# Kernel optimization log

Hardware: AMD Instinct MI355X
Metric: run time of the kernel (lower is better)

Reference implementation:

```python
import jax, jax.numpy as jnp
import numpy as np

V, D, H, L_GNN = 50000, 256, 256, 4
B, NODES_PER_G, L, OUT = 16, 4000, 512, 256
N = B * NODES_PER_G            # 64000 total nodes
E = N * 16                     # 1,024,000 edges (avg degree 16)


def setup_inputs() -> dict:
    key = jax.random.key(0)
    ks = jax.random.split(key, 14)
    s = 0.02  # param init scale
    # per-graph local indices, offset into the flat node array (mirrors the
    # indices[...] + sum(x_len[:i]) reconstruction in the torch code)
    local = jax.random.randint(ks[3], (B, L), 0, NODES_PER_G)
    offsets = (jnp.arange(B, dtype=jnp.int32) * NODES_PER_G)[:, None]
    return {
        "x": jax.random.randint(ks[0], (N,), 0, V, dtype=jnp.int32),
        "edge_index": jax.random.randint(ks[1], (2, E), 0, N, dtype=jnp.int32),
        "edge_weight": jax.random.uniform(ks[2], (E,), jnp.float32),
        "gather_idx": (local + offsets).astype(jnp.int32),
        "mask": jnp.ones((B, L), dtype=bool),
        "encoder_embed": jax.random.normal(ks[4], (B, L, H), jnp.float32),
        "emb": jax.random.normal(ks[5], (V, D), jnp.float32) * s,
        "ggc_w": jax.random.normal(ks[6], (L_GNN, H, H), jnp.float32) * s,
        "w_ih": jax.random.normal(ks[7], (3 * H, H), jnp.float32) * s,
        "w_hh": jax.random.normal(ks[8], (3 * H, H), jnp.float32) * s,
        "b_ih": jnp.zeros((3 * H,), jnp.float32),
        "b_hh": jnp.zeros((3 * H,), jnp.float32),
        "out_w": jax.random.normal(ks[9], (OUT, 2 * H), jnp.float32) * s,
        "out_b": jnp.zeros((OUT,), jnp.float32),
    }


def _gru_cell(m, h, w_ih, w_hh, b_ih, b_hh):
    # torch.nn.GRUCell, gate order (r, z, n)
    gi = m @ w_ih.T + b_ih          # [N, 3H]
    gh = h @ w_hh.T + b_hh
    i_r, i_z, i_n = jnp.split(gi, 3, axis=-1)
    h_r, h_z, h_n = jnp.split(gh, 3, axis=-1)
    r = jax.nn.sigmoid(i_r + h_r)
    z = jax.nn.sigmoid(i_z + h_z)
    n = jnp.tanh(i_n + r * h_n)
    return (1.0 - z) * n + z * h


def reference(x, edge_index, edge_weight, gather_idx, mask, encoder_embed,
              emb, ggc_w, w_ih, w_hh, b_ih, b_hh, out_w, out_b):
    src, dst = edge_index[0], edge_index[1]  # PyG: aggregate x_j at target i
    h = emb[x]                                # [N, H] (dropout=0 -> identity)
    for i in range(L_GNN):                    # GatedGraphConv
        m = h @ ggc_w[i]                      # [N, H]
        msg = m[src] * edge_weight[:, None]   # [E, H]
        agg = jax.ops.segment_sum(msg, dst, num_segments=N)
        h = _gru_cell(agg, h, w_ih, w_hh, b_ih, b_hh)
    # gather per-graph node outputs and zero-pad to max_node_len
    out = h[gather_idx] * mask[:, :, None].astype(h.dtype)  # [B, L, H]
    out = jnp.concatenate([out, encoder_embed], axis=-1)    # [B, L, 2H]
    return out @ out_w.T + out_b                            # [B, L, OUT]
```

## Files before the change

kernel.cpp:

```cpp
#include <hip/hip_runtime.h>
#include <hip/hip_bf16.h>

typedef __hip_bfloat16 bf16;
typedef unsigned short u16;
typedef __attribute__((ext_vector_type(8))) short s8v;
typedef __attribute__((ext_vector_type(4))) float f4v;

#define MFMA16(a, b, c) __builtin_amdgcn_mfma_f32_16x16x32_bf16((a), (b), (c), 0, 0, 0)

__device__ __forceinline__ float b2f(bf16 v) { return __bfloat162float(v); }
__device__ __forceinline__ float sigm(float x) {
  return __builtin_amdgcn_rcpf(1.0f + __expf(-x));
}
__device__ __forceinline__ float ftanh(float x) {
  return __builtin_fmaf(2.f, sigm(2.f * x), -1.f);
}
__device__ __forceinline__ float u2f(u16 u) {
  union { float f; unsigned int i; } v; v.i = ((unsigned int)u) << 16; return v.f;
}
__device__ __forceinline__ u16 f2u(float f) {
  bf16 b = __float2bfloat16(f);
  union { bf16 b; u16 u; } v; v.b = b; return v.u;
}

__device__ __forceinline__ void gl16(void* lds, const void* g) {
  __builtin_amdgcn_global_load_lds(
      (const __attribute__((address_space(1))) unsigned int*)g,
      (__attribute__((address_space(3))) unsigned int*)lds, 16, 0, 0);
}

__global__ __launch_bounds__(256) void k_cast4(const float* __restrict__ s0,
                                               const float* __restrict__ s1,
                                               const float* __restrict__ s2,
                                               const float* __restrict__ s3,
                                               bf16* __restrict__ d0,
                                               bf16* __restrict__ d1,
                                               bf16* __restrict__ d2,
                                               bf16* __restrict__ d3,
                                               int q0, int q1, int q2, int q3) {
  int i = blockIdx.x * 256 + threadIdx.x;
  const float* s; bf16* d;
  if (i < q0)            { s = s0; d = d0; }
  else if ((i -= q0) < q1) { s = s1; d = d1; }
  else if ((i -= q1) < q2) { s = s2; d = d2; }
  else if ((i -= q2) < q3) { s = s3; d = d3; }
  else return;
  float4 v = *(const float4*)(s + (size_t)i * 4);
  ushort4 o;
  o.x = f2u(v.x); o.y = f2u(v.y); o.z = f2u(v.z); o.w = f2u(v.w);
  *(ushort4*)((u16*)d + (size_t)i * 4) = o;
}

__global__ __launch_bounds__(256) void k_embed(const int* __restrict__ x,
                                               const float* __restrict__ emb,
                                               bf16* __restrict__ h, int N, int H) {
  int idx = blockIdx.x * 256 + threadIdx.x;
  int hq = H >> 2;
  if (idx >= N * hq) return;
  int n = idx / hq, c4 = idx - n * hq;
  float4 v = *(const float4*)(emb + (size_t)x[n] * H + c4 * 4);
  ushort4 o;
  o.x = f2u(v.x); o.y = f2u(v.y); o.z = f2u(v.z); o.w = f2u(v.w);
  *(ushort4*)((u16*)h + (size_t)idx * 4) = o;
}

__global__ __launch_bounds__(256) void k_cat(const bf16* __restrict__ h,
                                             const int* __restrict__ gidx,
                                             const float* __restrict__ enc,
                                             bf16* __restrict__ catA, int BL, int H) {
  int i = blockIdx.x * 256 + threadIdx.x;
  if (i >= BL * 2 * H) return;
  int r = i / (2 * H), k = i - r * 2 * H;
  catA[i] = (k < H) ? h[(size_t)gidx[r] * H + k]
                    : __float2bfloat16(enc[(size_t)r * H + (k - H)]);
}

__global__ __launch_bounds__(256) void k_zero_i32(int* __restrict__ p, int n) {
  int i = blockIdx.x * 256 + threadIdx.x;
  if (i < n) p[i] = 0;
}
__global__ __launch_bounds__(256) void k_hist(const int* __restrict__ ei,
                                              int* __restrict__ deg, int E) {
  int e = blockIdx.x * 256 + threadIdx.x;
  if (e < E) atomicAdd(&deg[ei[E + e]], 1);
}

__global__ __launch_bounds__(256) void k_scan1(const int* __restrict__ deg,
                                               int* __restrict__ bsum, int N) {
  int t = threadIdx.x;
  int i = blockIdx.x * 256 + t;
  int v = (i < N) ? deg[i] : 0;
#pragma unroll
  for (int o = 32; o > 0; o >>= 1) v += __shfl_down(v, o, 64);
  __shared__ int ws[4];
  if ((t & 63) == 0) ws[t >> 6] = v;
  __syncthreads();
  if (t == 0) bsum[blockIdx.x] = ws[0] + ws[1] + ws[2] + ws[3];
}
__global__ __launch_bounds__(256) void k_scan2(const int* __restrict__ bsum,
                                               int* __restrict__ boff, int nb) {
  __shared__ int s[256];
  int t = threadIdx.x;
  int carry = 0;
  for (int base = 0; base < nb; base += 256) {
    int v = (base + t < nb) ? bsum[base + t] : 0;
    s[t] = v;
    __syncthreads();
    for (int o = 1; o < 256; o <<= 1) {
      int u = (t >= o) ? s[t - o] : 0;
      __syncthreads();
      s[t] += u;
      __syncthreads();
    }
    if (base + t < nb) boff[base + t] = carry + s[t] - v;
    carry += s[255];
    __syncthreads();
  }
}
__global__ __launch_bounds__(256) void k_scan3(const int* __restrict__ deg,
                                               const int* __restrict__ boff,
                                               int* __restrict__ rowptr,
                                               int* __restrict__ cursor, int N) {
  __shared__ int s[256];
  int t = threadIdx.x;
  int i = blockIdx.x * 256 + t;
  int v = (i < N) ? deg[i] : 0;
  s[t] = v;
  __syncthreads();
  for (int o = 1; o < 256; o <<= 1) {
    int u = (t >= o) ? s[t - o] : 0;
    __syncthreads();
    s[t] += u;
    __syncthreads();
  }
  int ex = boff[blockIdx.x] + s[t] - v;
  if (i < N) { rowptr[i] = ex; cursor[i] = ex; }
  if (i == N - 1) rowptr[N] = ex + v;
}

__global__ __launch_bounds__(256) void k_fill(const int* __restrict__ ei,
                                              const float* __restrict__ ew,
                                              int* __restrict__ cursor,
                                              int2* __restrict__ ef, int E) {
  int e = blockIdx.x * 256 + threadIdx.x;
  if (e >= E) return;
  int d = ei[E + e];
  int pos = atomicAdd(&cursor[d], 1);
  ef[pos] = make_int2(ei[e], __float_as_int(ew[e]));
}

__global__ __launch_bounds__(256) void k_aggregate(const int* __restrict__ rowptr,
                                                   const int2* __restrict__ ef,
                                                   const bf16* __restrict__ hsrc,
                                                   bf16* __restrict__ sh,
                                                   int N, int H) {
  int wv = threadIdx.x >> 6, lane = threadIdx.x & 63;
  int d = blockIdx.x * 4 + wv;
  if (d >= N) return;
  int beg = rowptr[d], end = rowptr[d + 1];
  int half = lane >> 5;
  const u16* hp = (const u16*)hsrc;
  for (int c0 = (lane & 31) * 8; c0 < H; c0 += 256) {
    float f0 = 0.f, f1 = 0.f, f2 = 0.f, f3 = 0.f;
    float f4 = 0.f, f5 = 0.f, f6 = 0.f, f7 = 0.f;
    int i = beg;
    for (; i + 8 <= end; i += 8) {
      int2 eA = ef[i + half],     eB = ef[i + 2 + half];
      int2 eC = ef[i + 4 + half], eD = ef[i + 6 + half];
      float wA = __int_as_float(eA.y), wB = __int_as_float(eB.y);
      float wC = __int_as_float(eC.y), wD = __int_as_float(eD.y);
      s8v rA = *(const s8v*)(hp + (size_t)eA.x * H + c0);
      s8v rB = *(const s8v*)(hp + (size_t)eB.x * H + c0);
      s8v rC = *(const s8v*)(hp + (size_t)eC.x * H + c0);
      s8v rD = *(const s8v*)(hp + (size_t)eD.x * H + c0);
      f0 += wA * u2f((u16)rA[0]) + wB * u2f((u16)rB[0]) + wC * u2f((u16)rC[0]) + wD * u2f((u16)rD[0]);
      f1 += wA * u2f((u16)rA[1]) + wB * u2f((u16)rB[1]) + wC * u2f((u16)rC[1]) + wD * u2f((u16)rD[1]);
      f2 += wA * u2f((u16)rA[2]) + wB * u2f((u16)rB[2]) + wC * u2f((u16)rC[2]) + wD * u2f((u16)rD[2]);
      f3 += wA * u2f((u16)rA[3]) + wB * u2f((u16)rB[3]) + wC * u2f((u16)rC[3]) + wD * u2f((u16)rD[3]);
      f4 += wA * u2f((u16)rA[4]) + wB * u2f((u16)rB[4]) + wC * u2f((u16)rC[4]) + wD * u2f((u16)rD[4]);
      f5 += wA * u2f((u16)rA[5]) + wB * u2f((u16)rB[5]) + wC * u2f((u16)rC[5]) + wD * u2f((u16)rD[5]);
      f6 += wA * u2f((u16)rA[6]) + wB * u2f((u16)rB[6]) + wC * u2f((u16)rC[6]) + wD * u2f((u16)rD[6]);
      f7 += wA * u2f((u16)rA[7]) + wB * u2f((u16)rB[7]) + wC * u2f((u16)rC[7]) + wD * u2f((u16)rD[7]);
    }
    for (; i + 2 <= end; i += 2) {
      int2 eA = ef[i + half];
      float wA = __int_as_float(eA.y);
      s8v rA = *(const s8v*)(hp + (size_t)eA.x * H + c0);
      f0 += wA * u2f((u16)rA[0]); f1 += wA * u2f((u16)rA[1]);
      f2 += wA * u2f((u16)rA[2]); f3 += wA * u2f((u16)rA[3]);
      f4 += wA * u2f((u16)rA[4]); f5 += wA * u2f((u16)rA[5]);
      f6 += wA * u2f((u16)rA[6]); f7 += wA * u2f((u16)rA[7]);
    }
    if (i < end && half == 0) {
      int2 eA = ef[i];
      float wA = __int_as_float(eA.y);
      s8v rA = *(const s8v*)(hp + (size_t)eA.x * H + c0);
      f0 += wA * u2f((u16)rA[0]); f1 += wA * u2f((u16)rA[1]);
      f2 += wA * u2f((u16)rA[2]); f3 += wA * u2f((u16)rA[3]);
      f4 += wA * u2f((u16)rA[4]); f5 += wA * u2f((u16)rA[5]);
      f6 += wA * u2f((u16)rA[6]); f7 += wA * u2f((u16)rA[7]);
    }
    f0 += __shfl_xor(f0, 32); f1 += __shfl_xor(f1, 32);
    f2 += __shfl_xor(f2, 32); f3 += __shfl_xor(f3, 32);
    f4 += __shfl_xor(f4, 32); f5 += __shfl_xor(f5, 32);
    f6 += __shfl_xor(f6, 32); f7 += __shfl_xor(f7, 32);
    if (half == 0) {
      s8v o;
      o[0] = (short)f2u(f0); o[1] = (short)f2u(f1);
      o[2] = (short)f2u(f2); o[3] = (short)f2u(f3);
      o[4] = (short)f2u(f4); o[5] = (short)f2u(f5);
      o[6] = (short)f2u(f6); o[7] = (short)f2u(f7);
      *(s8v*)((u16*)sh + (size_t)d * H + c0) = o;
    }
  }
}

template <int OUT_F32>
__global__ __launch_bounds__(256) void k_gemm(const bf16* __restrict__ A,
                                              const bf16* __restrict__ Bt,
                                              void* __restrict__ Cv,
                                              const float* __restrict__ bias,
                                              int M, int K, int Nc,
                                              size_t sBt, size_t sC) {
  __shared__ short As[128][40];
  __shared__ short Bs[64][40];
  int gm = blockIdx.x * 128, gn = blockIdx.y * 64;
  Bt += (size_t)blockIdx.z * sBt;
  size_t zc = (size_t)blockIdx.z * sC;
  int tid = threadIdx.x, w = tid >> 6, lane = tid & 63;
  int l15 = lane & 15, koff = (lane >> 4) * 8;
  f4v acc[2][4];
#pragma unroll
  for (int i = 0; i < 2; i++)
#pragma unroll
    for (int j = 0; j < 4; j++) acc[i][j] = (f4v)0.f;

  for (int kt = 0; kt < K; kt += 32) {
#pragma unroll
    for (int c = 0; c < 2; c++) {
      int ch = tid + c * 256;
      int row = ch >> 2, seg = ch & 3;
      *(float4*)&As[row][seg * 8] =
          *(const float4*)(A + (size_t)(gm + row) * K + kt + seg * 8);
    }
    {
      int row = tid >> 2, seg = tid & 3;
      *(float4*)&Bs[row][seg * 8] =
          *(const float4*)(Bt + (size_t)(gn + row) * K + kt + seg * 8);
    }
    __syncthreads();
    s8v af[2], bf[4];
#pragma unroll
    for (int rt = 0; rt < 2; rt++) af[rt] = *(const s8v*)&As[w * 32 + rt * 16 + l15][koff];
#pragma unroll
    for (int ct = 0; ct < 4; ct++) bf[ct] = *(const s8v*)&Bs[ct * 16 + l15][koff];
#pragma unroll
    for (int rt = 0; rt < 2; rt++)
#pragma unroll
      for (int ct = 0; ct < 4; ct++) acc[rt][ct] = MFMA16(af[rt], bf[ct], acc[rt][ct]);
    __syncthreads();
  }
#pragma unroll
  for (int rt = 0; rt < 2; rt++)
#pragma unroll
    for (int ct = 0; ct < 4; ct++)
#pragma unroll
      for (int r = 0; r < 4; r++) {
        int row = gm + w * 32 + rt * 16 + (lane >> 4) * 4 + r;
        int col = gn + ct * 16 + l15;
        float v = acc[rt][ct][r];
        if (OUT_F32) ((float*)Cv)[zc + (size_t)row * Nc + col] = v + bias[col];
        else         ((bf16*)Cv)[zc + (size_t)row * Nc + col] = __float2bfloat16(v);
      }
}

#define GRU_STAGE(Aarr, Harr, Barr, kt)                   \
  {                                                       \
    gl16(&Aarr[tid * 8],            Ap  + (kt));          \
    gl16(&Aarr[2048 + tid * 8],     Ap  + rstep + (kt));  \
    gl16(&Harr[tid * 8],            Hp  + (kt));          \
    gl16(&Harr[2048 + tid * 8],     Hp  + rstep + (kt));  \
    gl16(&Barr[tid * 8],            BiP + (kt));          \
    gl16(&Barr[2048 + tid * 8],     BiP + HH + (kt));     \
    gl16(&Barr[2 * 2048 + tid * 8], BiP + 2 * HH + (kt)); \
    gl16(&Barr[3 * 2048 + tid * 8], BhP + (kt));          \
    gl16(&Barr[4 * 2048 + tid * 8], BhP + HH + (kt));     \
    gl16(&Barr[5 * 2048 + tid * 8], BhP + 2 * HH + (kt)); \
  }

#define GRU_COMPUTE(Aarr, Harr, Barr)                                       \
  {                                                                         \
    s8v fa[2], fh[2];                                                       \
    _Pragma("unroll")                                                       \
    for (int rt = 0; rt < 2; rt++) {                                        \
      fa[rt] = *(const s8v*)&Aarr[(w * 32 + rt * 16 + l15) * 32 + koff];    \
      fh[rt] = *(const s8v*)&Harr[(w * 32 + rt * 16 + l15) * 32 + koff];    \
    }                                                                       \
    _Pragma("unroll")                                                       \
    for (int ct = 0; ct < 4; ct++) {                                        \
      int brow = (ct * 16 + l15) * 32 + koff;                               \
      s8v bRi = *(const s8v*)&Barr[brow];                                   \
      s8v bZi = *(const s8v*)&Barr[2048 + brow];                            \
      s8v bNi = *(const s8v*)&Barr[2 * 2048 + brow];                        \
      s8v bRh = *(const s8v*)&Barr[3 * 2048 + brow];                        \
      s8v bZh = *(const s8v*)&Barr[4 * 2048 + brow];                        \
      s8v bNh = *(const s8v*)&Barr[5 * 2048 + brow];                        \
      _Pragma("unroll")                                                     \
      for (int rt = 0; rt < 2; rt++) {                                      \
        accR[rt][ct]  = MFMA16(fa[rt], bRi, accR[rt][ct]);                  \
        accR[rt][ct]  = MFMA16(fh[rt], bRh, accR[rt][ct]);                  \
        accZ[rt][ct]  = MFMA16(fa[rt], bZi, accZ[rt][ct]);                  \
        accZ[rt][ct]  = MFMA16(fh[rt], bZh, accZ[rt][ct]);                  \
        accNi[rt][ct] = MFMA16(fa[rt], bNi, accNi[rt][ct]);                 \
        accNh[rt][ct] = MFMA16(fh[rt], bNh, accNh[rt][ct]);                 \
      }                                                                     \
    }                                                                       \
  }

__global__ __launch_bounds__(256, 2) void k_gru_mfma(const bf16* __restrict__ Ash,
                                                     const bf16* __restrict__ Ah,
                                                     const bf16* __restrict__ Wi,
                                                     const bf16* __restrict__ Wh,
                                                     const float* __restrict__ bi,
                                                     const float* __restrict__ bh,
                                                     bf16* __restrict__ hn,
                                                     int M, int H) {
  __shared__ __align__(16) short Aa0[128 * 32], Aa1[128 * 32];
  __shared__ __align__(16) short Hs0[128 * 32], Hs1[128 * 32];
  __shared__ __align__(16) short Bs0[6 * 64 * 32], Bs1[6 * 64 * 32];

  int nwgx = H >> 6;
  int nwg = gridDim.x;
  int bid = blockIdx.x;
  int wg = bid;
  if ((nwg & 7) == 0) { int cpx = nwg >> 3; wg = (bid & 7) * cpx + (bid >> 3); }
  int gcol = (wg % nwgx) * 64;
  int gm = (wg / nwgx) * 128;

  int tid = threadIdx.x, w = tid >> 6, lane = tid & 63;
  int l15 = lane & 15, koff = (lane >> 4) * 8;
  f4v accR[2][4], accZ[2][4], accNi[2][4], accNh[2][4];
#pragma unroll
  for (int rt = 0; rt < 2; rt++)
#pragma unroll
    for (int ct = 0; ct < 4; ct++) {
      accR[rt][ct] = (f4v)0.f; accZ[rt][ct] = (f4v)0.f;
      accNi[rt][ct] = (f4v)0.f; accNh[rt][ct] = (f4v)0.f;
    }

  int arow = tid >> 2, aseg = tid & 3;
  const bf16* Ap  = Ash + (size_t)(gm + arow) * H + aseg * 8;
  const bf16* Hp  = Ah  + (size_t)(gm + arow) * H + aseg * 8;
  const bf16* BiP = Wi  + (size_t)(gcol + arow) * H + aseg * 8;
  const bf16* BhP = Wh  + (size_t)(gcol + arow) * H + aseg * 8;
  size_t HH = (size_t)H * H;
  size_t rstep = (size_t)64 * H;

  int nk = H >> 5;
  GRU_STAGE(Aa0, Hs0, Bs0, 0);
  __syncthreads();
  for (int t = 0; t < nk; t += 2) {
    int kt = t << 5;
    if (t + 1 < nk) GRU_STAGE(Aa1, Hs1, Bs1, kt + 32);
    GRU_COMPUTE(Aa0, Hs0, Bs0);
    __syncthreads();
    if (t + 2 < nk) GRU_STAGE(Aa0, Hs0, Bs0, kt + 64);
    if (t + 1 < nk) GRU_COMPUTE(Aa1, Hs1, Bs1);
    __syncthreads();
  }

#pragma unroll
  for (int ct = 0; ct < 4; ct++) {
    int col = gcol + ct * 16 + l15;
    float br  = bi[col] + bh[col];
    float bz  = bi[H + col] + bh[H + col];
    float bin = bi[2 * H + col], bhn = bh[2 * H + col];
#pragma unroll
    for (int rt = 0; rt < 2; rt++)
#pragma unroll
      for (int r = 0; r < 4; r++) {
        int row = gm + w * 32 + rt * 16 + (lane >> 4) * 4 + r;
        float rr = sigm(accR[rt][ct][r] + br);
        float zz = sigm(accZ[rt][ct][r] + bz);
        float nn = ftanh(accNi[rt][ct][r] + bin + rr * (accNh[rt][ct][r] + bhn));
        float hv = b2f(Ah[(size_t)row * H + col]);
        hn[(size_t)row * H + col] = __float2bfloat16((1.f - zz) * nn + zz * hv);
      }
  }
}

static inline size_t alg(size_t x) { return (x + 255) & ~(size_t)255; }
static inline int cdiv(int a, int b) { return (a + b - 1) / b; }

extern "C" void kernel_launch(void* const* d_in, const int* in_sizes, int n_in,
                              void* d_out, int out_size, void* d_ws, size_t ws_size,
                              hipStream_t stream) {
  (void)out_size; (void)ws_size;
  int s = (n_in >= 14) ? 0 : -1;
  const int*   x     = (const int*)d_in[0];
  const int*   ei    = (const int*)d_in[1];
  const float* ew    = (const float*)d_in[2];
  const int*   gidx  = (const int*)d_in[3];
  const float* enc   = (const float*)d_in[5 + s];
  const float* emb   = (const float*)d_in[6 + s];
  const float* ggcw  = (const float*)d_in[7 + s];
  const float* w_ih  = (const float*)d_in[8 + s];
  const float* w_hh  = (const float*)d_in[9 + s];
  const float* b_ih  = (const float*)d_in[10 + s];
  const float* b_hh  = (const float*)d_in[11 + s];
  const float* out_w = (const float*)d_in[12 + s];
  const float* out_b = (const float*)d_in[13 + s];
  float* out = (float*)d_out;

  int N   = in_sizes[0];
  int E   = in_sizes[2];
  int BL  = in_sizes[3];
  int H   = in_sizes[5 + s] / BL;
  int LG  = in_sizes[7 + s] / (H * H);
  int OUT = in_sizes[12 + s] / (2 * H);

  size_t nh = (size_t)N * H;
  size_t hh3 = (size_t)3 * H * H;
  int nb = cdiv(N, 256);
  char* p = (char*)d_ws;
  size_t off = 0;
  bf16* wihB  = (bf16*)(p + off); off = alg(off + hh3 * 2);
  bf16* whhB  = (bf16*)(p + off); off = alg(off + hh3 * 2);
  bf16* outwB = (bf16*)(p + off); off = alg(off + (size_t)OUT * 2 * H * 2);
  bf16* ggcwB = (bf16*)(p + off); off = alg(off + (size_t)LG * H * H * 2);
  bf16* Ucomb = (bf16*)(p + off); off = alg(off + (size_t)LG * hh3 * 2);
  bf16* hA    = (bf16*)(p + off); off = alg(off + nh * 2);
  bf16* hB    = (bf16*)(p + off); off = alg(off + nh * 2);
  bf16* shB   = (bf16*)(p + off); off = alg(off + nh * 2);
  bf16* catA  = (bf16*)(p + off); off = alg(off + (size_t)BL * 2 * H * 2);
  int* deg    = (int*)(p + off);  off = alg(off + (size_t)N * 4);
  int* rowptr = (int*)(p + off);  off = alg(off + (size_t)(N + 1) * 4);
  int* cursor = (int*)(p + off);  off = alg(off + (size_t)N * 4);
  int2* ef    = (int2*)(p + off); off = alg(off + (size_t)E * 8);
  int* bsum   = (int*)(p + off);  off = alg(off + (size_t)nb * 4);
  int* boff   = (int*)(p + off);  off = alg(off + (size_t)nb * 4);

  int q0 = (int)(hh3 >> 2), q1 = q0, q2 = (OUT * 2 * H) >> 2,
      q3 = (LG * H * H) >> 2;
  k_cast4<<<cdiv(q0 + q1 + q2 + q3, 256), 256, 0, stream>>>(
      w_ih, w_hh, out_w, ggcw, wihB, whhB, outwB, ggcwB, q0, q1, q2, q3);
  k_gemm<0><<<dim3(3 * H / 128, H / 64, LG), 256, 0, stream>>>(
      wihB, ggcwB, Ucomb, nullptr, 3 * H, H, H, (size_t)H * H, hh3);

  k_embed<<<cdiv(N * (H >> 2), 256), 256, 0, stream>>>(x, emb, hA, N, H);
  k_zero_i32<<<cdiv(N, 256), 256, 0, stream>>>(deg, N);
  k_hist<<<cdiv(E, 256), 256, 0, stream>>>(ei, deg, E);
  k_scan1<<<nb, 256, 0, stream>>>(deg, bsum, N);
  k_scan2<<<1, 256, 0, stream>>>(bsum, boff, nb);
  k_scan3<<<nb, 256, 0, stream>>>(deg, boff, rowptr, cursor, N);
  k_fill<<<cdiv(E, 256), 256, 0, stream>>>(ei, ew, cursor, ef, E);

  bf16* h = hA;
  bf16* hn = hB;
  for (int l = 0; l < LG; l++) {
    k_aggregate<<<cdiv(N, 4), 256, 0, stream>>>(rowptr, ef, h, shB, N, H);
    k_gru_mfma<<<dim3((H / 64) * (N / 128)), 256, 0, stream>>>(
        shB, h, Ucomb + (size_t)l * hh3, whhB, b_ih, b_hh, hn, N, H);
    bf16* t = h; h = hn; hn = t;
  }
  k_cat<<<cdiv(BL * 2 * H, 256), 256, 0, stream>>>(h, gidx, enc, catA, BL, H);
  k_gemm<1><<<dim3(BL / 128, OUT / 64, 1), 256, 0, stream>>>(
      catA, outwB, out, out_b, BL, 2 * H, OUT, 0, 0);
}
```

Before: 822.8 us.

## Fuse embed, weight cast and degree zeroing; partition CSR atomics by dst range

Merges the embedding gather, the weight casts and the degree-buffer zeroing into one prep kernel, removing two launches. The histogram and fill kernels now use a fixed grid of 2048 blocks split into 8 destination ranges. Each block scans its slice of the edge list but only issues atomics for destinations in its own range. The aim is to localise atomic traffic to a slice of deg and cursor so it stays in cache, at the cost of each edge index being read 8 times.

New measurement: 795.1 us. 1.03x faster.

```diff
diff --git a/kernel.cpp b/kernel.cpp
--- a/kernel.cpp
+++ b/kernel.cpp
@@ -29,39 +29,46 @@
       (__attribute__((address_space(3))) unsigned int*)lds, 16, 0, 0);
 }
 
-__global__ __launch_bounds__(256) void k_cast4(const float* __restrict__ s0,
-                                               const float* __restrict__ s1,
-                                               const float* __restrict__ s2,
-                                               const float* __restrict__ s3,
-                                               bf16* __restrict__ d0,
-                                               bf16* __restrict__ d1,
-                                               bf16* __restrict__ d2,
-                                               bf16* __restrict__ d3,
-                                               int q0, int q1, int q2, int q3) {
+__global__ __launch_bounds__(256) void k_prep(const int* __restrict__ x,
+                                              const float* __restrict__ emb,
+                                              bf16* __restrict__ h,
+                                              const float* __restrict__ s0,
+                                              const float* __restrict__ s1,
+                                              const float* __restrict__ s2,
+                                              const float* __restrict__ s3,
+                                              bf16* __restrict__ d0,
+                                              bf16* __restrict__ d1,
+                                              bf16* __restrict__ d2,
+                                              bf16* __restrict__ d3,
+                                              int q0, int q1, int q2, int q3,
+                                              int4* __restrict__ degz,
+                                              int N, int H, int nz) {
   int i = blockIdx.x * 256 + threadIdx.x;
+  int hq = H >> 2;
+  int nEmb = N * hq;
+  if (i < nEmb) {
+    int n = i / hq, c4 = i - n * hq;
+    float4 v = *(const float4*)(emb + (size_t)x[n] * H + c4 * 4);
+    ushort4 o;
+    o.x = f2u(v.x); o.y = f2u(v.y); o.z = f2u(v.z); o.w = f2u(v.w);
+    *(ushort4*)((u16*)h + (size_t)i * 4) = o;
+    return;
+  }
+  i -= nEmb;
   const float* s; bf16* d;
   if (i < q0)            { s = s0; d = d0; }
   else if ((i -= q0) < q1) { s = s1; d = d1; }
   else if ((i -= q1) < q2) { s = s2; d = d2; }
   else if ((i -= q2) < q3) { s = s3; d = d3; }
-  else return;
+  else {
+    i -= q3;
+    if (i < nz) degz[i] = make_int4(0, 0, 0, 0);
+    return;
+  }
   float4 v = *(const float4*)(s + (size_t)i * 4);
   ushort4 o;
   o.x = f2u(v.x); o.y = f2u(v.y); o.z = f2u(v.z); o.w = f2u(v.w);
   *(ushort4*)((u16*)d + (size_t)i * 4) = o;
-}
-
-__global__ __launch_bounds__(256) void k_embed(const int* __restrict__ x,
-                                               const float* __restrict__ emb,
-                                               bf16* __restrict__ h, int N, int H) {
-  int idx = blockIdx.x * 256 + threadIdx.x;
-  int hq = H >> 2;
-  if (idx >= N * hq) return;
-  int n = idx / hq, c4 = idx - n * hq;
-  float4 v = *(const float4*)(emb + (size_t)x[n] * H + c4 * 4);
-  ushort4 o;
-  o.x = f2u(v.x); o.y = f2u(v.y); o.z = f2u(v.z); o.w = f2u(v.w);
-  *(ushort4*)((u16*)h + (size_t)idx * 4) = o;
 }
 
 __global__ __launch_bounds__(256) void k_cat(const bf16* __restrict__ h,
@@ -75,14 +82,16 @@
                     : __float2bfloat16(enc[(size_t)r * H + (k - H)]);
 }
 
-__global__ __launch_bounds__(256) void k_zero_i32(int* __restrict__ p, int n) {
-  int i = blockIdx.x * 256 + threadIdx.x;
-  if (i < n) p[i] = 0;
-}
 __global__ __launch_bounds__(256) void k_hist(const int* __restrict__ ei,
-                                              int* __restrict__ deg, int E) {
-  int e = blockIdx.x * 256 + threadIdx.x;
-  if (e < E) atomicAdd(&deg[ei[E + e]], 1);
+                                              int* __restrict__ deg, int E, int N) {
+  int range = blockIdx.x & 7;
+  int seg = (N + 7) >> 3;
+  int lo = range * seg, hi = min(N, lo + seg);
+  int nb = gridDim.x >> 3, bslot = blockIdx.x >> 3;
+  for (int e = bslot * 256 + threadIdx.x; e < E; e += nb * 256) {
+    int d = ei[E + e];
+    if (d >= lo && d < hi) atomicAdd(&deg[d], 1);
+  }
 }
 
 __global__ __launch_bounds__(256) void k_scan1(const int* __restrict__ deg,
@@ -141,12 +150,18 @@
 __global__ __launch_bounds__(256) void k_fill(const int* __restrict__ ei,
                                               const float* __restrict__ ew,
                                               int* __restrict__ cursor,
-                                              int2* __restrict__ ef, int E) {
-  int e = blockIdx.x * 256 + threadIdx.x;
-  if (e >= E) return;
-  int d = ei[E + e];
-  int pos = atomicAdd(&cursor[d], 1);
-  ef[pos] = make_int2(ei[e], __float_as_int(ew[e]));
+                                              int2* __restrict__ ef, int E, int N) {
+  int range = blockIdx.x & 7;
+  int seg = (N + 7) >> 3;
+  int lo = range * seg, hi = min(N, lo + seg);
+  int nb = gridDim.x >> 3, bslot = blockIdx.x >> 3;
+  for (int e = bslot * 256 + threadIdx.x; e < E; e += nb * 256) {
+    int d = ei[E + e];
+    if (d >= lo && d < hi) {
+      int pos = atomicAdd(&cursor[d], 1);
+      ef[pos] = make_int2(ei[e], __float_as_int(ew[e]));
+    }
+  }
 }
 
 __global__ __launch_bounds__(256) void k_aggregate(const int* __restrict__ rowptr,
@@ -433,7 +448,7 @@
   bf16* hB    = (bf16*)(p + off); off = alg(off + nh * 2);
   bf16* shB   = (bf16*)(p + off); off = alg(off + nh * 2);
   bf16* catA  = (bf16*)(p + off); off = alg(off + (size_t)BL * 2 * H * 2);
-  int* deg    = (int*)(p + off);  off = alg(off + (size_t)N * 4);
+  int* deg    = (int*)(p + off);  off = alg(off + (size_t)cdiv(N, 4) * 16);
   int* rowptr = (int*)(p + off);  off = alg(off + (size_t)(N + 1) * 4);
   int* cursor = (int*)(p + off);  off = alg(off + (size_t)N * 4);
   int2* ef    = (int2*)(p + off); off = alg(off + (size_t)E * 8);
@@ -442,18 +457,19 @@
 
   int q0 = (int)(hh3 >> 2), q1 = q0, q2 = (OUT * 2 * H) >> 2,
       q3 = (LG * H * H) >> 2;
-  k_cast4<<<cdiv(q0 + q1 + q2 + q3, 256), 256, 0, stream>>>(
-      w_ih, w_hh, out_w, ggcw, wihB, whhB, outwB, ggcwB, q0, q1, q2, q3);
+  int nz = cdiv(N, 4);
+  int prep_total = N * (H >> 2) + q0 + q1 + q2 + q3 + nz;
+  k_prep<<<cdiv(prep_total, 256), 256, 0, stream>>>(
+      x, emb, hA, w_ih, w_hh, out_w, ggcw, wihB, whhB, outwB, ggcwB,
+      q0, q1, q2, q3, (int4*)deg, N, H, nz);
   k_gemm<0><<<dim3(3 * H / 128, H / 64, LG), 256, 0, stream>>>(
       wihB, ggcwB, Ucomb, nullptr, 3 * H, H, H, (size_t)H * H, hh3);
 
-  k_embed<<<cdiv(N * (H >> 2), 256), 256, 0, stream>>>(x, emb, hA, N, H);
-  k_zero_i32<<<cdiv(N, 256), 256, 0, stream>>>(deg, N);
-  k_hist<<<cdiv(E, 256), 256, 0, stream>>>(ei, deg, E);
+  k_hist<<<2048, 256, 0, stream>>>(ei, deg, E, N);
   k_scan1<<<nb, 256, 0, stream>>>(deg, bsum, N);
   k_scan2<<<1, 256, 0, stream>>>(bsum, boff, nb);
   k_scan3<<<nb, 256, 0, stream>>>(deg, boff, rowptr, cursor, N);
-  k_fill<<<cdiv(E, 256), 256, 0, stream>>>(ei, ew, cursor, ef, E);
+  k_fill<<<2048, 256, 0, stream>>>(ei, ew, cursor, ef, E, N);
 
   bf16* h = hA;
   bf16* hn = hB;
```
